# Kernel tuning notes

Hardware: AMD Instinct MI355X
Metric: run time of the kernel (lower is better)

## Reference

```python
import jax, jax.numpy as jnp
import numpy as np

B, T, I, H, L = 64, 512, 256, 512, 2


def setup_inputs() -> dict:
    key = jax.random.key(0)
    ks = jax.random.split(key, 9)
    std = 1.0 / np.sqrt(H)  # matches reset_parameters uniform(-std, std)
    u = lambda k, shape: jax.random.uniform(k, shape, jnp.float32, -std, std)
    return {
        "x": jax.random.normal(ks[0], (B, T, I), jnp.float32),
        "w_xh0": u(ks[1], (4 * H, I)),  "b_xh0": u(ks[2], (4 * H,)),
        "w_hh0": u(ks[3], (4 * H, H)), "b_hh0": u(ks[4], (4 * H,)),
        "w_xh1": u(ks[5], (4 * H, H)), "b_xh1": u(ks[6], (4 * H,)),
        "w_hh1": u(ks[7], (4 * H, H)), "b_hh1": u(ks[8], (4 * H,)),
    }


def _cell(x, h, c, Wx, bx, Wh, bh):
    # gates = xh(x) + hh(h); chunk order: input, forget, cell, output
    gates = x @ Wx.T + bx + h @ Wh.T + bh
    i, f, g, o = jnp.split(gates, 4, axis=1)
    cy = c * jax.nn.sigmoid(f) + jax.nn.sigmoid(i) * jnp.tanh(g)
    hy = jax.nn.sigmoid(o) * jnp.tanh(cy)
    return hy, cy


def reference(x, w_xh0, b_xh0, w_hh0, b_hh0, w_xh1, b_xh1, w_hh1, b_hh1):
    Bx, Tx, _ = x.shape
    Hx = w_hh0.shape[1]
    params = [(w_xh0, b_xh0, w_hh0, b_hh0), (w_xh1, b_xh1, w_hh1, b_hh1)]
    h0 = jnp.zeros((len(params), Bx, Hx), x.dtype)
    c0 = jnp.zeros((len(params), Bx, Hx), x.dtype)

    def step(carry, xt):
        h, c = carry
        inp = xt
        hs, cs = [], []
        for l, (Wx, bx, Wh, bh) in enumerate(params):
            hy, cy = _cell(inp, h[l], c[l], Wx, bx, Wh, bh)
            hs.append(hy)
            cs.append(cy)
            inp = hy  # dropout p=0.0 -> identity
        return (jnp.stack(hs), jnp.stack(cs)), inp

    (hT, cT), outs = jax.lax.scan(step, (h0, c0), jnp.swapaxes(x, 0, 1))
    return jnp.swapaxes(outs, 0, 1), (hT, cT)
```

## Files before the change

kernel.cpp:

```cpp
#include <hip/hip_runtime.h>
#include <stdint.h>

#define Bn 64
#define Tn 512
#define In 256
#define Hn 512
#define NBLK 64
#define OUT_HT 16777216
#define OUT_CT 16842752
#define LDS_BYTES 131072
#define SLOT_ELEMS (Bn * Hn)
#define CNT_BYTES 16384


typedef __attribute__((ext_vector_type(8))) short bf16x8;
typedef __attribute__((ext_vector_type(4))) float f32x4;
typedef unsigned long long u64;

__device__ __forceinline__ unsigned short f2bf(float f) {
    unsigned u = __float_as_uint(f);
    return (unsigned short)((u + 0x7fffu + ((u >> 16) & 1u)) >> 16);
}
__device__ __forceinline__ float sigm(float v) { return 1.0f / (1.0f + __expf(-v)); }
__device__ __forceinline__ float tanhv(float v) { float e = __expf(2.0f * v); return 1.0f - 2.0f / (e + 1.0f); }

__device__ __forceinline__ void stg_coh(unsigned short* p, unsigned short v) {
    __hip_atomic_store(p, v, __ATOMIC_RELAXED, __HIP_MEMORY_SCOPE_AGENT);
}
__device__ __forceinline__ int ld_cnt(const int* p) {
    return __hip_atomic_load(p, __ATOMIC_RELAXED, __HIP_MEMORY_SCOPE_AGENT);
}
__device__ __forceinline__ void st_flag(int* p, int v) {
    __hip_atomic_store(p, v, __ATOMIC_RELAXED, __HIP_MEMORY_SCOPE_AGENT);
}
__device__ __forceinline__ void wait32(const int* p) {
    while (ld_cnt(p) < 32) { }
}
__device__ __forceinline__ bf16x8 asbf(f32x4 v) {
    union { f32x4 f; bf16x8 h; } u; u.f = v; return u.h;
}

#define GLD16(A, VA)                                                   \
  asm volatile(                                                        \
    "global_load_dwordx4 %0,  %16, off offset:0 sc0 sc1\n\t"          \
    "global_load_dwordx4 %1,  %16, off offset:64 sc0 sc1\n\t"         \
    "global_load_dwordx4 %2,  %16, off offset:128 sc0 sc1\n\t"        \
    "global_load_dwordx4 %3,  %16, off offset:192 sc0 sc1\n\t"        \
    "global_load_dwordx4 %4,  %16, off offset:256 sc0 sc1\n\t"        \
    "global_load_dwordx4 %5,  %16, off offset:320 sc0 sc1\n\t"        \
    "global_load_dwordx4 %6,  %16, off offset:384 sc0 sc1\n\t"        \
    "global_load_dwordx4 %7,  %16, off offset:448 sc0 sc1\n\t"        \
    "global_load_dwordx4 %8,  %16, off offset:512 sc0 sc1\n\t"        \
    "global_load_dwordx4 %9,  %16, off offset:576 sc0 sc1\n\t"        \
    "global_load_dwordx4 %10, %16, off offset:640 sc0 sc1\n\t"        \
    "global_load_dwordx4 %11, %16, off offset:704 sc0 sc1\n\t"        \
    "global_load_dwordx4 %12, %16, off offset:768 sc0 sc1\n\t"        \
    "global_load_dwordx4 %13, %16, off offset:832 sc0 sc1\n\t"        \
    "global_load_dwordx4 %14, %16, off offset:896 sc0 sc1\n\t"        \
    "global_load_dwordx4 %15, %16, off offset:960 sc0 sc1\n\t"        \
    "s_waitcnt vmcnt(0)"                                               \
    : "=&v"(A[0]), "=&v"(A[1]), "=&v"(A[2]), "=&v"(A[3]),              \
      "=&v"(A[4]), "=&v"(A[5]), "=&v"(A[6]), "=&v"(A[7]),              \
      "=&v"(A[8]), "=&v"(A[9]), "=&v"(A[10]), "=&v"(A[11]),            \
      "=&v"(A[12]), "=&v"(A[13]), "=&v"(A[14]), "=&v"(A[15])           \
    : "v"(VA) : "memory")

#define GLD32(A, B, VA, VB)                                            \
  asm volatile(                                                        \
    "global_load_dwordx4 %0,  %32, off offset:0 sc0 sc1\n\t"          \
    "global_load_dwordx4 %1,  %32, off offset:64 sc0 sc1\n\t"         \
    "global_load_dwordx4 %2,  %32, off offset:128 sc0 sc1\n\t"        \
    "global_load_dwordx4 %3,  %32, off offset:192 sc0 sc1\n\t"        \
    "global_load_dwordx4 %4,  %32, off offset:256 sc0 sc1\n\t"        \
    "global_load_dwordx4 %5,  %32, off offset:320 sc0 sc1\n\t"        \
    "global_load_dwordx4 %6,  %32, off offset:384 sc0 sc1\n\t"        \
    "global_load_dwordx4 %7,  %32, off offset:448 sc0 sc1\n\t"        \
    "global_load_dwordx4 %8,  %32, off offset:512 sc0 sc1\n\t"        \
    "global_load_dwordx4 %9,  %32, off offset:576 sc0 sc1\n\t"        \
    "global_load_dwordx4 %10, %32, off offset:640 sc0 sc1\n\t"        \
    "global_load_dwordx4 %11, %32, off offset:704 sc0 sc1\n\t"        \
    "global_load_dwordx4 %12, %32, off offset:768 sc0 sc1\n\t"        \
    "global_load_dwordx4 %13, %32, off offset:832 sc0 sc1\n\t"        \
    "global_load_dwordx4 %14, %32, off offset:896 sc0 sc1\n\t"        \
    "global_load_dwordx4 %15, %32, off offset:960 sc0 sc1\n\t"        \
    "global_load_dwordx4 %16, %33, off offset:0 sc0 sc1\n\t"          \
    "global_load_dwordx4 %17, %33, off offset:64 sc0 sc1\n\t"         \
    "global_load_dwordx4 %18, %33, off offset:128 sc0 sc1\n\t"        \
    "global_load_dwordx4 %19, %33, off offset:192 sc0 sc1\n\t"        \
    "global_load_dwordx4 %20, %33, off offset:256 sc0 sc1\n\t"        \
    "global_load_dwordx4 %21, %33, off offset:320 sc0 sc1\n\t"        \
    "global_load_dwordx4 %22, %33, off offset:384 sc0 sc1\n\t"        \
    "global_load_dwordx4 %23, %33, off offset:448 sc0 sc1\n\t"        \
    "global_load_dwordx4 %24, %33, off offset:512 sc0 sc1\n\t"        \
    "global_load_dwordx4 %25, %33, off offset:576 sc0 sc1\n\t"        \
    "global_load_dwordx4 %26, %33, off offset:640 sc0 sc1\n\t"        \
    "global_load_dwordx4 %27, %33, off offset:704 sc0 sc1\n\t"        \
    "global_load_dwordx4 %28, %33, off offset:768 sc0 sc1\n\t"        \
    "global_load_dwordx4 %29, %33, off offset:832 sc0 sc1\n\t"        \
    "global_load_dwordx4 %30, %33, off offset:896 sc0 sc1\n\t"        \
    "global_load_dwordx4 %31, %33, off offset:960 sc0 sc1\n\t"        \
    "s_waitcnt vmcnt(0)"                                               \
    : "=&v"(A[0]), "=&v"(A[1]), "=&v"(A[2]), "=&v"(A[3]),              \
      "=&v"(A[4]), "=&v"(A[5]), "=&v"(A[6]), "=&v"(A[7]),              \
      "=&v"(A[8]), "=&v"(A[9]), "=&v"(A[10]), "=&v"(A[11]),            \
      "=&v"(A[12]), "=&v"(A[13]), "=&v"(A[14]), "=&v"(A[15]),          \
      "=&v"(B[0]), "=&v"(B[1]), "=&v"(B[2]), "=&v"(B[3]),              \
      "=&v"(B[4]), "=&v"(B[5]), "=&v"(B[6]), "=&v"(B[7]),              \
      "=&v"(B[8]), "=&v"(B[9]), "=&v"(B[10]), "=&v"(B[11]),            \
      "=&v"(B[12]), "=&v"(B[13]), "=&v"(B[14]), "=&v"(B[15])           \
    : "v"(VA), "v"(VB) : "memory")

__global__ void lstm_prep(u64* __restrict__ z0, u64* __restrict__ z1,
                          int* __restrict__ cnt) {
    int tid = blockIdx.x * blockDim.x + threadIdx.x;
    if (tid < CNT_BYTES / 4) st_flag(cnt + tid, 0);
    for (int i = tid; i < SLOT_ELEMS / 4; i += gridDim.x * blockDim.x) {
        __hip_atomic_store(z0 + i, (u64)0, __ATOMIC_RELAXED, __HIP_MEMORY_SCOPE_AGENT);
        __hip_atomic_store(z1 + i, (u64)0, __ATOMIC_RELAXED, __HIP_MEMORY_SCOPE_AGENT);
    }
}

__launch_bounds__(256, 1)
__global__ void lstm_main(const float* __restrict__ x,
                          const float* __restrict__ wxh0, const float* __restrict__ whh0,
                          const float* __restrict__ wxh1, const float* __restrict__ whh1,
                          const float* __restrict__ bx0, const float* __restrict__ bh0,
                          const float* __restrict__ bx1, const float* __restrict__ bh1,
                          float* __restrict__ out,
                          unsigned short* __restrict__ h0b,
                          unsigned short* __restrict__ h1b,
                          int* __restrict__ cnt, int nslot) {
    extern __shared__ char smem[];
    const int layer = blockIdx.x >> 5;
    const int cb    = blockIdx.x & 31;
    const int wv    = threadIdx.x >> 6;
    const int lane  = threadIdx.x & 63;
    const int quad  = lane >> 4;
    const int ln    = lane & 15;
    const int row0  = wv << 4;
    const int colh  = (cb << 4) + ln;

    const int I0 = (layer == 0) ? 8 : 16;
    const int K0 = (layer == 0) ? In : Hn;
    const float* Wxs = (layer == 0) ? wxh0 : wxh1;
    const float* Whs = (layer == 0) ? whh0 : whh1;
    u64* sm64 = (u64*)smem;
    const int tot0 = I0 * 4 * 64;
    for (int c = threadIdx.x; c < tot0; c += 256) {
        int lc = c & 63, qg = (c >> 6) & 3, ii = c >> 8;
        const float* src = Wxs + (size_t)(qg * Hn + (cb << 4) + (lc & 15)) * K0
                               + ii * 32 + (lc >> 4) * 8;
        f32x4 s0 = *(const f32x4*)src;
        f32x4 s1 = *(const f32x4*)(src + 4);
        u64 lo = (u64)f2bf(s0[0]) | ((u64)f2bf(s0[1]) << 16) |
                 ((u64)f2bf(s0[2]) << 32) | ((u64)f2bf(s0[3]) << 48);
        u64 hi = (u64)f2bf(s1[0]) | ((u64)f2bf(s1[1]) << 16) |
                 ((u64)f2bf(s1[2]) << 32) | ((u64)f2bf(s1[3]) << 48);
        sm64[c * 2] = lo; sm64[c * 2 + 1] = hi;
    }
    const int hbase = tot0;
    for (int c = threadIdx.x; c < 16 * 4 * 64; c += 256) {
        int lc = c & 63, qg = (c >> 6) & 3, ii = c >> 8;
        const float* src = Whs + (size_t)(qg * Hn + (cb << 4) + (lc & 15)) * Hn
                               + ii * 32 + (lc >> 4) * 8;
        f32x4 s0 = *(const f32x4*)src;
        f32x4 s1 = *(const f32x4*)(src + 4);
        u64 lo = (u64)f2bf(s0[0]) | ((u64)f2bf(s0[1]) << 16) |
                 ((u64)f2bf(s0[2]) << 32) | ((u64)f2bf(s0[3]) << 48);
        u64 hi = (u64)f2bf(s1[0]) | ((u64)f2bf(s1[1]) << 16) |
                 ((u64)f2bf(s1[2]) << 32) | ((u64)f2bf(s1[3]) << 48);
        sm64[(hbase + c) * 2] = lo; sm64[(hbase + c) * 2 + 1] = hi;
    }
    __syncthreads();
    const bf16x8* bfr = (const bf16x8*)smem;

    float bias[4];
#pragma unroll
    for (int q = 0; q < 4; ++q) {
        int gc = q * Hn + colh;
        bias[q] = (layer == 0) ? (bx0[gc] + bh0[gc]) : (bx1[gc] + bh1[gc]);
    }

    const float* xrow0 = x + (size_t)(row0 + ln) * Tn * In + quad * 8;
    const int hoff = (row0 + ln) * Hn + quad * 8;

    const int* c0 = cnt + (0 * 4 + wv) * Tn;
    const int* c1 = cnt + (1 * 4 + wv) * Tn;
    int* pub = cnt + (layer * 4 + wv) * Tn;

    float c[4] = {0.f, 0.f, 0.f, 0.f};
    int rs = 0, wsl = 1;
    int gdone = -1;

    for (int t = 0; t < Tn; ++t) {
        f32x4 acc[4];
#pragma unroll
        for (int q = 0; q < 4; ++q) acc[q] = (f32x4){bias[q], bias[q], bias[q], bias[q]};

        if (layer == 0) {
            const float* xp = xrow0 + (size_t)t * In;
            f32x4 xr[16];
#pragma unroll
            for (int i = 0; i < 8; ++i) {
                xr[2 * i]     = *(const f32x4*)(xp + i * 32);
                xr[2 * i + 1] = *(const f32x4*)(xp + i * 32 + 4);
            }
            bf16x8 axc[8];
#pragma unroll
            for (int i = 0; i < 8; ++i) {
                f32x4 xa = xr[2 * i], xc = xr[2 * i + 1];
                axc[i][0] = (short)f2bf(xa[0]); axc[i][1] = (short)f2bf(xa[1]);
                axc[i][2] = (short)f2bf(xa[2]); axc[i][3] = (short)f2bf(xa[3]);
                axc[i][4] = (short)f2bf(xc[0]); axc[i][5] = (short)f2bf(xc[1]);
                axc[i][6] = (short)f2bf(xc[2]); axc[i][7] = (short)f2bf(xc[3]);
            }
#pragma unroll
            for (int i = 0; i < 8; ++i)
#pragma unroll
                for (int q = 0; q < 4; ++q)
                    acc[q] = __builtin_amdgcn_mfma_f32_16x16x32_bf16(
                        axc[i], bfr[(i * 4 + q) * 64 + lane], acc[q], 0, 0, 0);

            if (t > 0) wait32(c0 + (t - 1));
            {
                int g = t + 1 - nslot;
                if (g >= 0 && g > gdone) {
                    int probe = g + 32; if (probe > Tn - 1) probe = Tn - 1;
                    if (ld_cnt(c1 + probe) >= 32) gdone = probe;
                    else { wait32(c1 + g); gdone = g; }
                }
            }
            asm volatile("" ::: "memory");

            const unsigned short* hp = h0b + (size_t)rs * SLOT_ELEMS + hoff;
            f32x4 A[16];
            uint64_t va = (uint64_t)hp;
            GLD16(A, va);
#pragma unroll
            for (int i = 0; i < 16; ++i)
#pragma unroll
                for (int q = 0; q < 4; ++q)
                    acc[q] = __builtin_amdgcn_mfma_f32_16x16x32_bf16(
                        asbf(A[i]), bfr[hbase + (i * 4 + q) * 64 + lane], acc[q], 0, 0, 0);
        } else {
            wait32(c0 + t);
            if (t > 0) wait32(c1 + (t - 1));
            asm volatile("" ::: "memory");

            const unsigned short* p0 = h0b + (size_t)wsl * SLOT_ELEMS + hoff;
            const unsigned short* p1 = h1b + (size_t)rs  * SLOT_ELEMS + hoff;
            f32x4 A[16], Bv[16];
            uint64_t va = (uint64_t)p0, vb = (uint64_t)p1;
            GLD32(A, Bv, va, vb);
#pragma unroll
            for (int i = 0; i < 16; ++i)
#pragma unroll
                for (int q = 0; q < 4; ++q)
                    acc[q] = __builtin_amdgcn_mfma_f32_16x16x32_bf16(
                        asbf(A[i]), bfr[(i * 4 + q) * 64 + lane], acc[q], 0, 0, 0);
#pragma unroll
            for (int i = 0; i < 16; ++i)
#pragma unroll
                for (int q = 0; q < 4; ++q)
                    acc[q] = __builtin_amdgcn_mfma_f32_16x16x32_bf16(
                        asbf(Bv[i]), bfr[hbase + (i * 4 + q) * 64 + lane], acc[q], 0, 0, 0);
        }

        unsigned short* hw = ((layer == 0) ? h0b : h1b) + (size_t)wsl * SLOT_ELEMS;
#pragma unroll
        for (int r = 0; r < 4; ++r) {
            int row = row0 + quad * 4 + r;
            float ig = sigm(acc[0][r]);
            float fg = sigm(acc[1][r]);
            float gg = tanhv(acc[2][r]);
            float og = sigm(acc[3][r]);
            float cy = c[r] * fg + ig * gg;
            float hy = og * tanhv(cy);
            c[r] = cy;
            stg_coh(hw + row * Hn + colh, f2bf(hy));
            if (layer == 1) out[(size_t)row * (Tn * Hn) + (size_t)t * Hn + colh] = hy;
            if (t == Tn - 1) {
                out[OUT_HT + layer * (Bn * Hn) + row * Hn + colh] = hy;
                out[OUT_CT + layer * (Bn * Hn) + row * Hn + colh] = cy;
            }
        }

        asm volatile("s_waitcnt vmcnt(0)" ::: "memory");
        if (lane == 0)
            __hip_atomic_fetch_add(pub + t, 1, __ATOMIC_RELAXED, __HIP_MEMORY_SCOPE_AGENT);

        rs = wsl;
        wsl = (wsl + 1 == nslot) ? 0 : wsl + 1;
    }
}

extern "C" void kernel_launch(void* const* d_in, const int* in_sizes, int n_in,
                              void* d_out, int out_size, void* d_ws, size_t ws_size,
                              hipStream_t stream) {
    const float* x    = (const float*)d_in[0];
    const float* wxh0 = (const float*)d_in[1];
    const float* bxh0 = (const float*)d_in[2];
    const float* whh0 = (const float*)d_in[3];
    const float* bhh0 = (const float*)d_in[4];
    const float* wxh1 = (const float*)d_in[5];
    const float* bxh1 = (const float*)d_in[6];
    const float* whh1 = (const float*)d_in[7];
    const float* bhh1 = (const float*)d_in[8];
    float* out = (float*)d_out;

    char* ws = (char*)d_ws;
    int* cnt = (int*)ws;
    long nslot_l = (long)((ws_size - CNT_BYTES) / (2 * (size_t)SLOT_ELEMS * 2));
    int nslot = (int)(nslot_l < 3 ? 3 : (nslot_l > Tn + 1 ? Tn + 1 : nslot_l));
    unsigned short* h0b = (unsigned short*)(ws + CNT_BYTES);
    unsigned short* h1b = h0b + (size_t)nslot * SLOT_ELEMS;

    static int lds_attr_set = 0;
    if (!lds_attr_set) {
        hipFuncSetAttribute((const void*)lstm_main,
                            hipFuncAttributeMaxDynamicSharedMemorySize, LDS_BYTES);
        lds_attr_set = 1;
    }

    lstm_prep<<<dim3(32), dim3(256), 0, stream>>>((u64*)h0b, (u64*)h1b, cnt);

    lstm_main<<<dim3(NBLK), dim3(256), LDS_BYTES, stream>>>(
        x, wxh0, whh0, wxh1, whh1, bxh0, bhh0, bxh1, bhh1,
        out, h0b, h1b, cnt, nslot);
}
```

Baseline: 3.649 ms.

## Replace atomic step counters with per-block flags and pipeline h loads with MFMAs

Replaces the per-step atomic counter (32 fetch_adds polled until the count reaches 32) with one flag word per producer block, which the lanes of a wave poll in parallel and combine with __all. The layer-1 path now issues the layer-0 h load before waiting on the layer-1 dependency. Both paths consume loads in chunks with staged s_waitcnt so MFMAs start while the remaining loads are in flight. Output stores are moved after the flag publish to shorten the critical path. The cost is a larger flag region in the workspace, more polling traffic, and a bigger prep launch.

```diff
diff --git a/kernel.cpp b/kernel.cpp
--- a/kernel.cpp
+++ b/kernel.cpp
@@ -10,7 +10,8 @@
 #define OUT_CT 16842752
 #define LDS_BYTES 131072
 #define SLOT_ELEMS (Bn * Hn)
-#define CNT_BYTES 16384
+#define DONE_WORDS (2 * 4 * Tn * 32)
+#define DONE_BYTES (DONE_WORDS * 4)
 
 
 typedef __attribute__((ext_vector_type(8))) short bf16x8;
@@ -33,14 +34,11 @@
 __device__ __forceinline__ void st_flag(int* p, int v) {
     __hip_atomic_store(p, v, __ATOMIC_RELAXED, __HIP_MEMORY_SCOPE_AGENT);
 }
-__device__ __forceinline__ void wait32(const int* p) {
-    while (ld_cnt(p) < 32) { }
-}
 __device__ __forceinline__ bf16x8 asbf(f32x4 v) {
     union { f32x4 f; bf16x8 h; } u; u.f = v; return u.h;
 }
 
-#define GLD16(A, VA)                                                   \
+#define GLD16_ISSUE(A, VA)                                             \
   asm volatile(                                                        \
     "global_load_dwordx4 %0,  %16, off offset:0 sc0 sc1\n\t"          \
     "global_load_dwordx4 %1,  %16, off offset:64 sc0 sc1\n\t"         \
@@ -57,64 +55,24 @@
     "global_load_dwordx4 %12, %16, off offset:768 sc0 sc1\n\t"        \
     "global_load_dwordx4 %13, %16, off offset:832 sc0 sc1\n\t"        \
     "global_load_dwordx4 %14, %16, off offset:896 sc0 sc1\n\t"        \
-    "global_load_dwordx4 %15, %16, off offset:960 sc0 sc1\n\t"        \
-    "s_waitcnt vmcnt(0)"                                               \
+    "global_load_dwordx4 %15, %16, off offset:960 sc0 sc1"             \
     : "=&v"(A[0]), "=&v"(A[1]), "=&v"(A[2]), "=&v"(A[3]),              \
       "=&v"(A[4]), "=&v"(A[5]), "=&v"(A[6]), "=&v"(A[7]),              \
       "=&v"(A[8]), "=&v"(A[9]), "=&v"(A[10]), "=&v"(A[11]),            \
       "=&v"(A[12]), "=&v"(A[13]), "=&v"(A[14]), "=&v"(A[15])           \
     : "v"(VA) : "memory")
 
-#define GLD32(A, B, VA, VB)                                            \
-  asm volatile(                                                        \
-    "global_load_dwordx4 %0,  %32, off offset:0 sc0 sc1\n\t"          \
-    "global_load_dwordx4 %1,  %32, off offset:64 sc0 sc1\n\t"         \
-    "global_load_dwordx4 %2,  %32, off offset:128 sc0 sc1\n\t"        \
-    "global_load_dwordx4 %3,  %32, off offset:192 sc0 sc1\n\t"        \
-    "global_load_dwordx4 %4,  %32, off offset:256 sc0 sc1\n\t"        \
-    "global_load_dwordx4 %5,  %32, off offset:320 sc0 sc1\n\t"        \
-    "global_load_dwordx4 %6,  %32, off offset:384 sc0 sc1\n\t"        \
-    "global_load_dwordx4 %7,  %32, off offset:448 sc0 sc1\n\t"        \
-    "global_load_dwordx4 %8,  %32, off offset:512 sc0 sc1\n\t"        \
-    "global_load_dwordx4 %9,  %32, off offset:576 sc0 sc1\n\t"        \
-    "global_load_dwordx4 %10, %32, off offset:640 sc0 sc1\n\t"        \
-    "global_load_dwordx4 %11, %32, off offset:704 sc0 sc1\n\t"        \
-    "global_load_dwordx4 %12, %32, off offset:768 sc0 sc1\n\t"        \
-    "global_load_dwordx4 %13, %32, off offset:832 sc0 sc1\n\t"        \
-    "global_load_dwordx4 %14, %32, off offset:896 sc0 sc1\n\t"        \
-    "global_load_dwordx4 %15, %32, off offset:960 sc0 sc1\n\t"        \
-    "global_load_dwordx4 %16, %33, off offset:0 sc0 sc1\n\t"          \
-    "global_load_dwordx4 %17, %33, off offset:64 sc0 sc1\n\t"         \
-    "global_load_dwordx4 %18, %33, off offset:128 sc0 sc1\n\t"        \
-    "global_load_dwordx4 %19, %33, off offset:192 sc0 sc1\n\t"        \
-    "global_load_dwordx4 %20, %33, off offset:256 sc0 sc1\n\t"        \
-    "global_load_dwordx4 %21, %33, off offset:320 sc0 sc1\n\t"        \
-    "global_load_dwordx4 %22, %33, off offset:384 sc0 sc1\n\t"        \
-    "global_load_dwordx4 %23, %33, off offset:448 sc0 sc1\n\t"        \
-    "global_load_dwordx4 %24, %33, off offset:512 sc0 sc1\n\t"        \
-    "global_load_dwordx4 %25, %33, off offset:576 sc0 sc1\n\t"        \
-    "global_load_dwordx4 %26, %33, off offset:640 sc0 sc1\n\t"        \
-    "global_load_dwordx4 %27, %33, off offset:704 sc0 sc1\n\t"        \
-    "global_load_dwordx4 %28, %33, off offset:768 sc0 sc1\n\t"        \
-    "global_load_dwordx4 %29, %33, off offset:832 sc0 sc1\n\t"        \
-    "global_load_dwordx4 %30, %33, off offset:896 sc0 sc1\n\t"        \
-    "global_load_dwordx4 %31, %33, off offset:960 sc0 sc1\n\t"        \
-    "s_waitcnt vmcnt(0)"                                               \
-    : "=&v"(A[0]), "=&v"(A[1]), "=&v"(A[2]), "=&v"(A[3]),              \
-      "=&v"(A[4]), "=&v"(A[5]), "=&v"(A[6]), "=&v"(A[7]),              \
-      "=&v"(A[8]), "=&v"(A[9]), "=&v"(A[10]), "=&v"(A[11]),            \
-      "=&v"(A[12]), "=&v"(A[13]), "=&v"(A[14]), "=&v"(A[15]),          \
-      "=&v"(B[0]), "=&v"(B[1]), "=&v"(B[2]), "=&v"(B[3]),              \
-      "=&v"(B[4]), "=&v"(B[5]), "=&v"(B[6]), "=&v"(B[7]),              \
-      "=&v"(B[8]), "=&v"(B[9]), "=&v"(B[10]), "=&v"(B[11]),            \
-      "=&v"(B[12]), "=&v"(B[13]), "=&v"(B[14]), "=&v"(B[15])           \
-    : "v"(VA), "v"(VB) : "memory")
+#define VMW(n) do {                                                    \
+    asm volatile("s_waitcnt vmcnt(" #n ")" ::: "memory");              \
+    __builtin_amdgcn_sched_barrier(0);                                 \
+  } while (0)
 
 __global__ void lstm_prep(u64* __restrict__ z0, u64* __restrict__ z1,
-                          int* __restrict__ cnt) {
+                          int* __restrict__ dn) {
     int tid = blockIdx.x * blockDim.x + threadIdx.x;
-    if (tid < CNT_BYTES / 4) st_flag(cnt + tid, 0);
-    for (int i = tid; i < SLOT_ELEMS / 4; i += gridDim.x * blockDim.x) {
+    int stride = gridDim.x * blockDim.x;
+    for (int i = tid; i < DONE_WORDS; i += stride) st_flag(dn + i, 0);
+    for (int i = tid; i < SLOT_ELEMS / 4; i += stride) {
         __hip_atomic_store(z0 + i, (u64)0, __ATOMIC_RELAXED, __HIP_MEMORY_SCOPE_AGENT);
         __hip_atomic_store(z1 + i, (u64)0, __ATOMIC_RELAXED, __HIP_MEMORY_SCOPE_AGENT);
     }
@@ -129,7 +87,7 @@
                           float* __restrict__ out,
                           unsigned short* __restrict__ h0b,
                           unsigned short* __restrict__ h1b,
-                          int* __restrict__ cnt, int nslot) {
+                          int* __restrict__ done, int nslot) {
     extern __shared__ char smem[];
     const int layer = blockIdx.x >> 5;
     const int cb    = blockIdx.x & 31;
@@ -184,9 +142,10 @@
     const float* xrow0 = x + (size_t)(row0 + ln) * Tn * In + quad * 8;
     const int hoff = (row0 + ln) * Hn + quad * 8;
 
-    const int* c0 = cnt + (0 * 4 + wv) * Tn;
-    const int* c1 = cnt + (1 * 4 + wv) * Tn;
-    int* pub = cnt + (layer * 4 + wv) * Tn;
+    const int lm = lane & 31;
+    const int* d0 = done + ((0 * 4 + wv) * Tn) * 32 + lm;
+    const int* d1 = done + ((1 * 4 + wv) * Tn) * 32 + lm;
+    int* pub = done + ((layer * 4 + wv) * Tn) * 32 + cb;
 
     float c[4] = {0.f, 0.f, 0.f, 0.f};
     int rs = 0, wsl = 1;
@@ -221,45 +180,126 @@
                     acc[q] = __builtin_amdgcn_mfma_f32_16x16x32_bf16(
                         axc[i], bfr[(i * 4 + q) * 64 + lane], acc[q], 0, 0, 0);
 
-            if (t > 0) wait32(c0 + (t - 1));
             {
                 int g = t + 1 - nslot;
                 if (g >= 0 && g > gdone) {
                     int probe = g + 32; if (probe > Tn - 1) probe = Tn - 1;
-                    if (ld_cnt(c1 + probe) >= 32) gdone = probe;
-                    else { wait32(c1 + g); gdone = g; }
+                    if (__all(ld_cnt(d1 + probe * 32) > 0)) gdone = probe;
+                    else {
+                        const int* gp = d1 + g * 32;
+                        while (!__all(ld_cnt(gp) > 0)) __builtin_amdgcn_s_sleep(4);
+                        gdone = g;
+                    }
                 }
+            }
+            if (t > 0) {
+                const int* p = d0 + (t - 1) * 32;
+                while (!__all(ld_cnt(p) > 0)) { }
             }
             asm volatile("" ::: "memory");
 
             const unsigned short* hp = h0b + (size_t)rs * SLOT_ELEMS + hoff;
             f32x4 A[16];
             uint64_t va = (uint64_t)hp;
-            GLD16(A, va);
-#pragma unroll
-            for (int i = 0; i < 16; ++i)
+            GLD16_ISSUE(A, va);
+            VMW(12);
+#pragma unroll
+            for (int i = 0; i < 4; ++i)
+#pragma unroll
+                for (int q = 0; q < 4; ++q)
+                    acc[q] = __builtin_amdgcn_mfma_f32_16x16x32_bf16(
+                        asbf(A[i]), bfr[hbase + (i * 4 + q) * 64 + lane], acc[q], 0, 0, 0);
+            VMW(8);
+#pragma unroll
+            for (int i = 4; i < 8; ++i)
+#pragma unroll
+                for (int q = 0; q < 4; ++q)
+                    acc[q] = __builtin_amdgcn_mfma_f32_16x16x32_bf16(
+                        asbf(A[i]), bfr[hbase + (i * 4 + q) * 64 + lane], acc[q], 0, 0, 0);
+            VMW(4);
+#pragma unroll
+            for (int i = 8; i < 12; ++i)
+#pragma unroll
+                for (int q = 0; q < 4; ++q)
+                    acc[q] = __builtin_amdgcn_mfma_f32_16x16x32_bf16(
+                        asbf(A[i]), bfr[hbase + (i * 4 + q) * 64 + lane], acc[q], 0, 0, 0);
+            VMW(0);
+#pragma unroll
+            for (int i = 12; i < 16; ++i)
 #pragma unroll
                 for (int q = 0; q < 4; ++q)
                     acc[q] = __builtin_amdgcn_mfma_f32_16x16x32_bf16(
                         asbf(A[i]), bfr[hbase + (i * 4 + q) * 64 + lane], acc[q], 0, 0, 0);
         } else {
-            wait32(c0 + t);
-            if (t > 0) wait32(c1 + (t - 1));
+            {
+                const int* p = d0 + t * 32;
+                while (!__all(ld_cnt(p) > 0)) { }
+            }
             asm volatile("" ::: "memory");
-
             const unsigned short* p0 = h0b + (size_t)wsl * SLOT_ELEMS + hoff;
-            const unsigned short* p1 = h1b + (size_t)rs  * SLOT_ELEMS + hoff;
             f32x4 A[16], Bv[16];
-            uint64_t va = (uint64_t)p0, vb = (uint64_t)p1;
-            GLD32(A, Bv, va, vb);
-#pragma unroll
-            for (int i = 0; i < 16; ++i)
+            uint64_t va = (uint64_t)p0;
+            GLD16_ISSUE(A, va);
+            if (t > 0) {
+                const int* p = d1 + (t - 1) * 32;
+                while (!__all(ld_cnt(p) > 0)) { }
+            }
+            asm volatile("" ::: "memory");
+            const unsigned short* p1 = h1b + (size_t)rs * SLOT_ELEMS + hoff;
+            uint64_t vb = (uint64_t)p1;
+            GLD16_ISSUE(Bv, vb);
+            VMW(28);
+#pragma unroll
+            for (int i = 0; i < 4; ++i)
 #pragma unroll
                 for (int q = 0; q < 4; ++q)
                     acc[q] = __builtin_amdgcn_mfma_f32_16x16x32_bf16(
                         asbf(A[i]), bfr[(i * 4 + q) * 64 + lane], acc[q], 0, 0, 0);
-#pragma unroll
-            for (int i = 0; i < 16; ++i)
+            VMW(24);
+#pragma unroll
+            for (int i = 4; i < 8; ++i)
+#pragma unroll
+                for (int q = 0; q < 4; ++q)
+                    acc[q] = __builtin_amdgcn_mfma_f32_16x16x32_bf16(
+                        asbf(A[i]), bfr[(i * 4 + q) * 64 + lane], acc[q], 0, 0, 0);
+            VMW(20);
+#pragma unroll
+            for (int i = 8; i < 12; ++i)
+#pragma unroll
+                for (int q = 0; q < 4; ++q)
+                    acc[q] = __builtin_amdgcn_mfma_f32_16x16x32_bf16(
+                        asbf(A[i]), bfr[(i * 4 + q) * 64 + lane], acc[q], 0, 0, 0);
+            VMW(16);
+#pragma unroll
+            for (int i = 12; i < 16; ++i)
+#pragma unroll
+                for (int q = 0; q < 4; ++q)
+                    acc[q] = __builtin_amdgcn_mfma_f32_16x16x32_bf16(
+                        asbf(A[i]), bfr[(i * 4 + q) * 64 + lane], acc[q], 0, 0, 0);
+            VMW(12);
+#pragma unroll
+            for (int i = 0; i < 4; ++i)
+#pragma unroll
+                for (int q = 0; q < 4; ++q)
+                    acc[q] = __builtin_amdgcn_mfma_f32_16x16x32_bf16(
+                        asbf(Bv[i]), bfr[hbase + (i * 4 + q) * 64 + lane], acc[q], 0, 0, 0);
+            VMW(8);
+#pragma unroll
+            for (int i = 4; i < 8; ++i)
+#pragma unroll
+                for (int q = 0; q < 4; ++q)
+                    acc[q] = __builtin_amdgcn_mfma_f32_16x16x32_bf16(
+                        asbf(Bv[i]), bfr[hbase + (i * 4 + q) * 64 + lane], acc[q], 0, 0, 0);
+            VMW(4);
+#pragma unroll
+            for (int i = 8; i < 12; ++i)
+#pragma unroll
+                for (int q = 0; q < 4; ++q)
+                    acc[q] = __builtin_amdgcn_mfma_f32_16x16x32_bf16(
+                        asbf(Bv[i]), bfr[hbase + (i * 4 + q) * 64 + lane], acc[q], 0, 0, 0);
+            VMW(0);
+#pragma unroll
+            for (int i = 12; i < 16; ++i)
 #pragma unroll
                 for (int q = 0; q < 4; ++q)
                     acc[q] = __builtin_amdgcn_mfma_f32_16x16x32_bf16(
@@ -267,6 +307,7 @@
         }
 
         unsigned short* hw = ((layer == 0) ? h0b : h1b) + (size_t)wsl * SLOT_ELEMS;
+        float hv[4];
 #pragma unroll
         for (int r = 0; r < 4; ++r) {
             int row = row0 + quad * 4 + r;
@@ -277,17 +318,27 @@
             float cy = c[r] * fg + ig * gg;
             float hy = og * tanhv(cy);
             c[r] = cy;
+            hv[r] = hy;
             stg_coh(hw + row * Hn + colh, f2bf(hy));
-            if (layer == 1) out[(size_t)row * (Tn * Hn) + (size_t)t * Hn + colh] = hy;
-            if (t == Tn - 1) {
-                out[OUT_HT + layer * (Bn * Hn) + row * Hn + colh] = hy;
-                out[OUT_CT + layer * (Bn * Hn) + row * Hn + colh] = cy;
-            }
         }
-
         asm volatile("s_waitcnt vmcnt(0)" ::: "memory");
-        if (lane == 0)
-            __hip_atomic_fetch_add(pub + t, 1, __ATOMIC_RELAXED, __HIP_MEMORY_SCOPE_AGENT);
+        if (lane == 0) st_flag(pub + t * 32, t + 1);
+
+        if (layer == 1) {
+#pragma unroll
+            for (int r = 0; r < 4; ++r) {
+                int row = row0 + quad * 4 + r;
+                out[(size_t)row * (Tn * Hn) + (size_t)t * Hn + colh] = hv[r];
+            }
+        }
+        if (t == Tn - 1) {
+#pragma unroll
+            for (int r = 0; r < 4; ++r) {
+                int row = row0 + quad * 4 + r;
+                out[OUT_HT + layer * (Bn * Hn) + row * Hn + colh] = hv[r];
+                out[OUT_CT + layer * (Bn * Hn) + row * Hn + colh] = c[r];
+            }
+        }
 
         rs = wsl;
         wsl = (wsl + 1 == nslot) ? 0 : wsl + 1;
@@ -309,10 +360,10 @@
     float* out = (float*)d_out;
 
     char* ws = (char*)d_ws;
-    int* cnt = (int*)ws;
-    long nslot_l = (long)((ws_size - CNT_BYTES) / (2 * (size_t)SLOT_ELEMS * 2));
+    int* done = (int*)ws;
+    long nslot_l = (long)((ws_size - DONE_BYTES) / (2 * (size_t)SLOT_ELEMS * 2));
     int nslot = (int)(nslot_l < 3 ? 3 : (nslot_l > Tn + 1 ? Tn + 1 : nslot_l));
-    unsigned short* h0b = (unsigned short*)(ws + CNT_BYTES);
+    unsigned short* h0b = (unsigned short*)(ws + DONE_BYTES);
     unsigned short* h1b = h0b + (size_t)nslot * SLOT_ELEMS;
 
     static int lds_attr_set = 0;
@@ -322,9 +373,9 @@
         lds_attr_set = 1;
     }
 
-    lstm_prep<<<dim3(32), dim3(256), 0, stream>>>((u64*)h0b, (u64*)h1b, cnt);
+    lstm_prep<<<dim3(256), dim3(256), 0, stream>>>((u64*)h0b, (u64*)h1b, done);
 
     lstm_main<<<dim3(NBLK), dim3(256), LDS_BYTES, stream>>>(
         x, wxh0, whh0, wxh1, whh1, bxh0, bhh0, bxh1, bhh1,
-        out, h0b, h1b, cnt, nslot);
-}
+        out, h0b, h1b, done, nslot);
+}
```

New measurement: 3.365 ms. 1.08x faster.
